# Kernel tuning notes

Hardware: AMD Instinct MI355X
Metric: run time of the kernel (lower is better)

Reference implementation:

```python
import jax, jax.numpy as jnp
import numpy as np

EPS = 1e-5
K = 20

def knn_idx(x, k):
    # x: (B, N, C) -> (B, N, k) indices of k nearest neighbors (negative sq-dist top-k, self included)
    sq = jnp.sum(x * x, axis=-1)                      # (B, N)
    inner = jnp.einsum('bnc,bmc->bnm', x, x)          # (B, N, N)
    neg_dist = 2.0 * inner - sq[:, :, None] - sq[:, None, :]
    _, idx = jax.lax.top_k(neg_dist, k)
    return idx

def edge_conv(x, w, g, b, m, v, k):
    # x: (B, N, C); w: (O, 2C); BN eval-mode params over O
    idx = knn_idx(x, k)                               # (B, N, k)
    nb = jax.vmap(lambda f, i: f[i])(x, idx)          # (B, N, k, C)
    ctr = x[:, :, None, :]
    e = jnp.concatenate([nb - ctr, jnp.broadcast_to(ctr, nb.shape)], axis=-1)  # (B,N,k,2C)
    h = jnp.einsum('bnkc,oc->bnko', e, w)
    h = (h - m) * jax.lax.rsqrt(v + EPS) * g + b
    h = jnp.where(h > 0, h, 0.2 * h)                  # LeakyReLU(0.2)
    return jnp.max(h, axis=2)                         # (B, N, O)

def conv1d_bn_relu(x, w, bias, g, bt, m, v):
    h = jnp.einsum('bnc,oc->bno', x, w) + bias
    h = (h - m) * jax.lax.rsqrt(v + EPS) * g + bt
    return jax.nn.relu(h)

def setup_inputs() -> dict:
    key = jax.random.key(0)
    ks = jax.random.split(key, 16)
    B, N = 2, 4096
    d = {'x': jax.random.normal(ks[0], (B, N, 3), dtype=jnp.float32)}
    dims = [(3, 64), (64, 64), (64, 128), (128, 256)]
    for i, (ci, co) in enumerate(dims, start=1):
        d[f'w{i}'] = jax.random.normal(ks[i], (co, 2 * ci), dtype=jnp.float32) * 0.05
        d[f'g{i}'] = jnp.ones((co,), jnp.float32)
        d[f'bt{i}'] = jnp.zeros((co,), jnp.float32)
        d[f'm{i}'] = jnp.zeros((co,), jnp.float32)
        d[f'v{i}'] = jnp.ones((co,), jnp.float32)
    head = [(512, 256), (256, 128)]
    for i, (ci, co) in enumerate(head, start=1):
        d[f'hw{i}'] = jax.random.normal(ks[8 + i], (co, ci), dtype=jnp.float32) * 0.05
        d[f'hb{i}'] = jnp.zeros((co,), jnp.float32)
        d[f'hg{i}'] = jnp.ones((co,), jnp.float32)
        d[f'hbt{i}'] = jnp.zeros((co,), jnp.float32)
        d[f'hm{i}'] = jnp.zeros((co,), jnp.float32)
        d[f'hv{i}'] = jnp.ones((co,), jnp.float32)
    d['hw3'] = jax.random.normal(ks[12], (1, 128), dtype=jnp.float32) * 0.05
    d['hb3'] = jnp.zeros((1,), jnp.float32)
    return d

def reference(x, w1, g1, bt1, m1, v1, w2, g2, bt2, m2, v2, w3, g3, bt3, m3, v3,
              w4, g4, bt4, m4, v4,
              hw1, hb1, hg1, hbt1, hm1, hv1, hw2, hb2, hg2, hbt2, hm2, hv2, hw3, hb3):
    x1 = edge_conv(x, w1, g1, bt1, m1, v1, K)   # (B, N, 64)
    x2 = edge_conv(x1, w2, g2, bt2, m2, v2, K)  # (B, N, 64)
    x3 = edge_conv(x2, w3, g3, bt3, m3, v3, K)  # (B, N, 128)
    x4 = edge_conv(x3, w4, g4, bt4, m4, v4, K)  # (B, N, 256)
    xc = jnp.concatenate([x1, x2, x3, x4], axis=-1)  # (B, N, 512)
    h = conv1d_bn_relu(xc, hw1, hb1, hg1, hbt1, hm1, hv1)
    h = conv1d_bn_relu(h, hw2, hb2, hg2, hbt2, hm2, hv2)
    out = jnp.einsum('bnc,oc->bno', h, hw3) + hb3    # (B, N, 1)
    return out[..., 0]                               # (B, N)
```

## Files before the change

kernel.cpp:

```cpp
#include <hip/hip_runtime.h>

#define NPTS 4096
#define EPSF 1e-5f

__device__ __forceinline__ unsigned f2u(float f) {
  unsigned b = __float_as_uint(f);
  return (b & 0x80000000u) ? ~b : (b | 0x80000000u);
}
__device__ __forceinline__ float u2f(unsigned u) {
  unsigned b = (u & 0x80000000u) ? (u & 0x7fffffffu) : ~u;
  return __uint_as_float(b);
}
__device__ __forceinline__ unsigned shflx(unsigned v, int j) {
  return (unsigned)__shfl_xor((int)v, j);
}
__device__ __forceinline__ unsigned long long shflx64(unsigned long long v, int j) {
  unsigned lo = (unsigned)__shfl_xor((int)(unsigned)(v & 0xffffffffull), j);
  unsigned hi = (unsigned)__shfl_xor((int)(unsigned)(v >> 32), j);
  return ((unsigned long long)hi << 32) | lo;
}

__device__ __forceinline__ unsigned sort64_u32(unsigned v, int lane) {
#pragma unroll
  for (int k = 2; k <= 64; k <<= 1) {
#pragma unroll
    for (int j = k >> 1; j >= 1; j >>= 1) {
      unsigned ov = shflx(v, j);
      bool kmin = ((lane & j) == 0) == ((lane & k) == 0);
      v = kmin ? (v < ov ? v : ov) : (v > ov ? v : ov);
    }
  }
  return v;
}

__device__ __forceinline__ void sort128_u32(unsigned& a, unsigned& b, int lane) {
#pragma unroll
  for (int k = 2; k <= 128; k <<= 1) {
#pragma unroll
    for (int j = k >> 1; j >= 1; j >>= 1) {
      if (j == 64) {
        unsigned mn = a < b ? a : b, mx = a < b ? b : a;
        a = mn; b = mx;
      } else {
        unsigned oa = shflx(a, j), ob = shflx(b, j);
        bool lower = (lane & j) == 0;
        bool asca, ascb;
        if (k == 128) { asca = true; ascb = true; }
        else if (k == 64) { asca = true; ascb = false; }
        else { asca = ((lane & k) == 0); ascb = asca; }
        a = (lower == asca) ? (a < oa ? a : oa) : (a > oa ? a : oa);
        b = (lower == ascb) ? (b < ob ? b : ob) : (b > ob ? b : ob);
      }
    }
  }
}

__device__ __forceinline__ unsigned long long sort64_u64(unsigned long long v, int lane) {
#pragma unroll
  for (int k = 2; k <= 64; k <<= 1) {
#pragma unroll
    for (int j = k >> 1; j >= 1; j >>= 1) {
      unsigned long long ov = shflx64(v, j);
      bool kmin = ((lane & j) == 0) == ((lane & k) == 0);
      v = kmin ? (v < ov ? v : ov) : (v > ov ? v : ov);
    }
  }
  return v;
}

__device__ __forceinline__ void sort128_u64(unsigned long long& a, unsigned long long& b,
                                            int lane) {
#pragma unroll
  for (int k = 2; k <= 128; k <<= 1) {
#pragma unroll
    for (int j = k >> 1; j >= 1; j >>= 1) {
      if (j == 64) {
        unsigned long long mn = a < b ? a : b, mx = a < b ? b : a;
        a = mn; b = mx;
      } else {
        unsigned long long oa = shflx64(a, j), ob = shflx64(b, j);
        bool lower = (lane & j) == 0;
        bool asca, ascb;
        if (k == 128) { asca = true; ascb = true; }
        else if (k == 64) { asca = true; ascb = false; }
        else { asca = ((lane & k) == 0); ascb = asca; }
        a = (lower == asca) ? (a < oa ? a : oa) : (a > oa ? a : oa);
        b = (lower == ascb) ? (b < ob ? b : ob) : (b > ob ? b : ob);
      }
    }
  }
}

__global__ void fold_edge_k(const float* __restrict__ w, const float* __restrict__ g,
                            const float* __restrict__ bt, const float* __restrict__ m,
                            const float* __restrict__ v, int O, int C,
                            float* __restrict__ wdf, float* __restrict__ wqf,
                            float* __restrict__ c0) {
  int t = blockIdx.x * 256 + threadIdx.x;
  if (t >= O * C) return;
  int o = t / C, c = t - o * C;
  float A = g[o] * (1.0f / sqrtf(v[o] + EPSF));
  float wd = w[o * 2 * C + c], wc = w[o * 2 * C + C + c];
  wdf[t] = A * wd;
  wqf[t] = A * (wc - wd);
  if (c == 0) c0[o] = bt[o] - m[o] * A;
}

__global__ void fold_head_k(const float* __restrict__ hw, const float* __restrict__ hb,
                            const float* __restrict__ hg, const float* __restrict__ hbt,
                            const float* __restrict__ hm, const float* __restrict__ hv,
                            int O, int C, float* __restrict__ hwf, float* __restrict__ cb) {
  int t = blockIdx.x * 256 + threadIdx.x;
  if (t >= O * C) return;
  int o = t / C, c = t - o * C;
  float A = hg[o] * (1.0f / sqrtf(hv[o] + EPSF));
  hwf[t] = A * hw[t];
  if (c == 0) cb[o] = (hb[o] - hm[o]) * A + hbt[o];
}

__global__ void sq_k(const float* __restrict__ X, int lda, int C,
                     float* __restrict__ sq, int nrows) {
  int r = blockIdx.x * 256 + threadIdx.x;
  if (r >= nrows) return;
  const float* p = X + (size_t)r * lda;
  float s = 0.f;
  for (int c = 0; c < C; ++c) s += p[c] * p[c];
  sq[r] = s;
}

__global__ void pq3_k(const float* __restrict__ x, const float* __restrict__ wdf,
                      const float* __restrict__ wqf, const float* __restrict__ c0,
                      float* __restrict__ P, float* __restrict__ Q) {
  int t = blockIdx.x * 256 + threadIdx.x;
  int r = t >> 6, o = t & 63;
  float x0 = x[r * 3], x1 = x[r * 3 + 1], x2 = x[r * 3 + 2];
  P[(size_t)r * 64 + o] = x0 * wdf[o * 3] + x1 * wdf[o * 3 + 1] + x2 * wdf[o * 3 + 2];
  Q[(size_t)r * 64 + o] = x0 * wqf[o * 3] + x1 * wqf[o * 3 + 1] + x2 * wqf[o * 3 + 2] + c0[o];
}

__global__ void dist3_all(const float* __restrict__ x, const float* __restrict__ sq,
                          float* __restrict__ D) {
  size_t t = (size_t)blockIdx.x * 256 + threadIdx.x;
  int mc = (int)(t & (NPTS - 1));
  int rg = (int)(t >> 12);
  int b = rg >> 12;
  int n = rg & (NPTS - 1);
  const float* xb = x + (size_t)b * NPTS * 3;
  const float* sqb = sq + (size_t)b * NPTS;
  float x0 = xb[n * 3], x1 = xb[n * 3 + 1], x2 = xb[n * 3 + 2];
  float y0 = xb[mc * 3], y1 = xb[mc * 3 + 1], y2 = xb[mc * 3 + 2];
  float inner = x0 * y0 + x1 * y1 + x2 * y2;
  D[(size_t)rg * NPTS + mc] = 2.0f * inner - sqb[n] - sqb[mc];
}

__global__ void dist3_k(const float* __restrict__ xb, const float* __restrict__ sqb,
                        float* __restrict__ D, int r0) {
  int t = blockIdx.x * 256 + threadIdx.x;
  int rl = t >> 12;
  int mc = t & (NPTS - 1);
  int n = r0 + rl;
  float x0 = xb[n * 3], x1 = xb[n * 3 + 1], x2 = xb[n * 3 + 2];
  float y0 = xb[mc * 3], y1 = xb[mc * 3 + 1], y2 = xb[mc * 3 + 2];
  float inner = x0 * y0 + x1 * y1 + x2 * y2;
  D[(size_t)rl * NPTS + mc] = 2.0f * inner - sqb[n] - sqb[mc];
}

__global__ __launch_bounds__(256) void dist_sym_k(
    const float* __restrict__ X0, int lda, int C,
    const float* __restrict__ sq0, float* __restrict__ D0) {
  int t = blockIdx.x;
  int bi = 0;
  while (t >= 32 - bi) { t -= 32 - bi; ++bi; }
  const int bj = bi + t;
  const int b = blockIdx.y;
  const float* X = X0 + (size_t)b * NPTS * lda;
  const float* sq = sq0 + (size_t)b * NPTS;
  float* D = D0 + (size_t)b * NPTS * NPTS;

  const int row0 = bi * 128, col0 = bj * 128;
  const int tid = threadIdx.x;
  const int tx = tid & 15, ty = tid >> 4;

  __shared__ float smem[4224];
  float* As = smem;
  float* Bs = smem + 2112;

  const int lr = tid >> 1;
  const int lc = (tid & 1) * 8;
  const float* Ap = X + (size_t)(row0 + lr) * lda + lc;
  const float* Bp = X + (size_t)(col0 + lr) * lda + lc;

  float acc[8][8] = {};
  for (int c0 = 0; c0 < C; c0 += 16) {
    float4 a0 = *(const float4*)(Ap + c0);
    float4 a1 = *(const float4*)(Ap + c0 + 4);
    float4 b0 = *(const float4*)(Bp + c0);
    float4 b1 = *(const float4*)(Bp + c0 + 4);
    __syncthreads();
    As[(lc + 0) * 132 + lr] = a0.x; As[(lc + 1) * 132 + lr] = a0.y;
    As[(lc + 2) * 132 + lr] = a0.z; As[(lc + 3) * 132 + lr] = a0.w;
    As[(lc + 4) * 132 + lr] = a1.x; As[(lc + 5) * 132 + lr] = a1.y;
    As[(lc + 6) * 132 + lr] = a1.z; As[(lc + 7) * 132 + lr] = a1.w;
    Bs[(lc + 0) * 132 + lr] = b0.x; Bs[(lc + 1) * 132 + lr] = b0.y;
    Bs[(lc + 2) * 132 + lr] = b0.z; Bs[(lc + 3) * 132 + lr] = b0.w;
    Bs[(lc + 4) * 132 + lr] = b1.x; Bs[(lc + 5) * 132 + lr] = b1.y;
    Bs[(lc + 6) * 132 + lr] = b1.z; Bs[(lc + 7) * 132 + lr] = b1.w;
    __syncthreads();
#pragma unroll
    for (int c = 0; c < 16; ++c) {
      float4 av0 = *(const float4*)&As[c * 132 + ty * 8];
      float4 av1 = *(const float4*)&As[c * 132 + ty * 8 + 4];
      float4 bv0 = *(const float4*)&Bs[c * 132 + tx * 8];
      float4 bv1 = *(const float4*)&Bs[c * 132 + tx * 8 + 4];
      float aa[8] = {av0.x, av0.y, av0.z, av0.w, av1.x, av1.y, av1.z, av1.w};
      float bb[8] = {bv0.x, bv0.y, bv0.z, bv0.w, bv1.x, bv1.y, bv1.z, bv1.w};
#pragma unroll
      for (int i = 0; i < 8; ++i)
#pragma unroll
        for (int j = 0; j < 8; ++j) acc[i][j] = fmaf(aa[i], bb[j], acc[i][j]);
    }
  }

  float rs[8], cs[8];
#pragma unroll
  for (int i = 0; i < 8; ++i) rs[i] = sq[row0 + ty * 8 + i];
#pragma unroll
  for (int j = 0; j < 8; ++j) cs[j] = sq[col0 + tx * 8 + j];

#pragma unroll
  for (int i = 0; i < 8; ++i) {
    const int row = row0 + ty * 8 + i;
    float vals[8];
#pragma unroll
    for (int j = 0; j < 8; ++j) vals[j] = (2.0f * acc[i][j] - rs[i]) - cs[j];
    *(float4*)&D[(size_t)row * NPTS + col0 + tx * 8] =
        make_float4(vals[0], vals[1], vals[2], vals[3]);
    *(float4*)&D[(size_t)row * NPTS + col0 + tx * 8 + 4] =
        make_float4(vals[4], vals[5], vals[6], vals[7]);
  }

  if (bi != bj) {
    for (int ch = 0; ch < 4; ++ch) {
      __syncthreads();
      if ((tx >> 2) == ch) {
#pragma unroll
        for (int j = 0; j < 8; ++j) {
          const int clocal = (tx & 3) * 8 + j;
#pragma unroll
          for (int i = 0; i < 8; ++i)
            smem[clocal * 129 + ty * 8 + i] = (2.0f * acc[i][j] - cs[j]) - rs[i];
        }
      }
      __syncthreads();
      const int cl = tid >> 3;
      const int seg = (tid & 7) * 16;
      float tv[16];
#pragma unroll
      for (int u = 0; u < 16; ++u) tv[u] = smem[cl * 129 + seg + u];
      const size_t mrow = (size_t)(col0 + ch * 32 + cl) * NPTS + row0 + seg;
#pragma unroll
      for (int q = 0; q < 4; ++q)
        *(float4*)&D[mrow + 4 * q] =
            make_float4(tv[4 * q], tv[4 * q + 1], tv[4 * q + 2], tv[4 * q + 3]);
    }
  }
}

template <int EPI>
__global__ __launch_bounds__(256) void gemm_nt(
    const float* __restrict__ A, int lda,
    const float* __restrict__ Bm, int ldb,
    float* __restrict__ Out, int ldo, int C,
    const float* __restrict__ sqA, const float* __restrict__ sqB,
    const float* __restrict__ bias) {
  __shared__ __align__(16) float As[16][68];
  __shared__ __align__(16) float Bs[16][68];
  const int tx = threadIdx.x, ty = threadIdx.y;
  const int tid = ty * 16 + tx;
  const int row0 = blockIdx.y * 64, col0 = blockIdx.x * 64;
  const int lr = tid >> 2;
  const int lc = (tid & 3) << 2;
  const float* Ap = A + (size_t)(row0 + lr) * lda + lc;
  const float* Bp = Bm + (size_t)(col0 + lr) * ldb + lc;
  float acc[4][4] = {};
  for (int c0 = 0; c0 < C; c0 += 16) {
    float4 av = *(const float4*)(Ap + c0);
    float4 bv = *(const float4*)(Bp + c0);
    As[lc + 0][lr] = av.x; As[lc + 1][lr] = av.y;
    As[lc + 2][lr] = av.z; As[lc + 3][lr] = av.w;
    Bs[lc + 0][lr] = bv.x; Bs[lc + 1][lr] = bv.y;
    Bs[lc + 2][lr] = bv.z; Bs[lc + 3][lr] = bv.w;
    __syncthreads();
#pragma unroll
    for (int c = 0; c < 16; ++c) {
      float4 a4 = *(const float4*)(&As[c][ty << 2]);
      float4 b4 = *(const float4*)(&Bs[c][tx << 2]);
      float aa[4] = {a4.x, a4.y, a4.z, a4.w};
      float bb[4] = {b4.x, b4.y, b4.z, b4.w};
#pragma unroll
      for (int i = 0; i < 4; ++i)
#pragma unroll
        for (int j = 0; j < 4; ++j) acc[i][j] = fmaf(aa[i], bb[j], acc[i][j]);
    }
    __syncthreads();
  }
  const int row = row0 + (ty << 2), col = col0 + (tx << 2);
#pragma unroll
  for (int i = 0; i < 4; ++i) {
    float vals[4];
#pragma unroll
    for (int j = 0; j < 4; ++j) {
      float va = acc[i][j];
      if (EPI == 0) vals[j] = va;
      else if (EPI == 1) vals[j] = va + bias[col + j];
      else if (EPI == 2) vals[j] = 2.0f * va - sqA[row + i] - sqB[col + j];
      else { float t = va + bias[col + j]; vals[j] = t > 0.f ? t : 0.f; }
    }
    *(float4*)(&Out[(size_t)(row + i) * ldo + col]) =
        make_float4(vals[0], vals[1], vals[2], vals[3]);
  }
}

__global__ __launch_bounds__(256) void topk_max_f32(
    const float* __restrict__ D, long long dStride,
    const float* __restrict__ P, const float* __restrict__ Q,
    float* __restrict__ Y, int ldy, int O, int bBase0, int r0) {
  const int tid = threadIdx.x;
  const int lane = tid & 63, wid = tid >> 6;
  const int nloc = blockIdx.x;
  const int n = r0 + nloc;
  const int bBase = bBase0 + blockIdx.y * NPTS;
  const float* drow = D + (size_t)blockIdx.y * (size_t)dStride + (size_t)nloc * NPTS;

  __shared__ unsigned wv[80];
  __shared__ unsigned ck[128];
  __shared__ int      ci[128];
  __shared__ int      cnt_s;
  __shared__ int      selm[20];
  __shared__ float    part[4 * 256];
  __shared__ float    fcv[80];
  __shared__ int      fcm[80];

  float v[16];
#pragma unroll
  for (int j = 0; j < 16; ++j) v[j] = drow[j * 256 + tid];

  float M = v[0];
#pragma unroll
  for (int j = 1; j < 16; ++j) M = fmaxf(M, v[j]);

  unsigned mk = sort64_u32(f2u(M), lane);

  if (tid == 0) cnt_s = 0;
  if (lane >= 44) wv[wid * 20 + (63 - lane)] = mk;
  __syncthreads();

  unsigned a0 = wv[lane];
  unsigned b0 = (lane < 16) ? wv[64 + lane] : 0u;
  sort128_u32(a0, b0, lane);
  unsigned T0k = (unsigned)__shfl((int)b0, 44);
  float T0f = u2f(T0k);

#pragma unroll
  for (int j = 0; j < 16; ++j) {
    bool pred = (v[j] >= T0f);
    unsigned long long m = __ballot(pred);
    int below = __popcll(m & ((1ull << lane) - 1ull));
    int cw = __popcll(m);
    int base = 0;
    if (lane == 0 && cw) base = atomicAdd(&cnt_s, cw);
    base = __shfl(base, 0);
    if (pred) {
      int pos = base + below;
      if (pos < 128) { ck[pos] = f2u(v[j]); ci[pos] = j * 256 + tid; }
    }
  }
  __syncthreads();
  const int cnt = cnt_s;

  if (cnt <= 128) {
    unsigned long long k0 = (lane < cnt)
        ? (((unsigned long long)ck[lane] << 32) | (unsigned)(~ci[lane])) : 0ull;
    if (cnt <= 64) {
      k0 = sort64_u64(k0, lane);
      if (wid == 0 && lane >= 44) selm[63 - lane] = (int)(~(unsigned)k0);
    } else {
      unsigned long long k1 = (64 + lane < cnt)
          ? (((unsigned long long)ck[64 + lane] << 32) | (unsigned)(~ci[64 + lane])) : 0ull;
      sort128_u64(k0, k1, lane);
      if (wid == 0 && lane >= 44) selm[63 - lane] = (int)(~(unsigned)k1);
    }
  } else {
    for (int it = 0; it < 20; ++it) {
      float bv = v[0]; int bj = 0;
#pragma unroll
      for (int j = 1; j < 16; ++j)
        if (v[j] > bv) { bv = v[j]; bj = j; }
      int bm = bj * 256 + tid;
#pragma unroll
      for (int off = 1; off < 64; off <<= 1) {
        float ov = __shfl_xor(bv, off);
        int om = __shfl_xor(bm, off);
        if (ov > bv || (ov == bv && om < bm)) { bv = ov; bm = om; }
      }
      if (lane == 0) { fcv[wid * 20 + it] = bv; fcm[wid * 20 + it] = bm; }
      if ((bm & 255) == tid) v[bm >> 8] = -3.0e38f;
    }
    __syncthreads();
    if (wid == 0) {
      float c0 = fcv[lane]; int m0 = fcm[lane];
      float c1 = (lane < 16) ? fcv[64 + lane] : -3.0e38f;
      int   m1 = (lane < 16) ? fcm[64 + lane] : 0x7fffffff;
      for (int it = 0; it < 20; ++it) {
        float bv; int bm, bs;
        if (c0 > c1 || (c0 == c1 && m0 < m1)) { bv = c0; bm = m0; bs = lane; }
        else { bv = c1; bm = m1; bs = 64 + lane; }
#pragma unroll
        for (int off = 1; off < 64; off <<= 1) {
          float ov = __shfl_xor(bv, off);
          int om = __shfl_xor(bm, off);
          int os = __shfl_xor(bs, off);
          if (ov > bv || (ov == bv && om < bm)) { bv = ov; bm = om; bs = os; }
        }
        if (lane == 0) selm[it] = bm;
        if (bs == lane) c0 = -3.0e38f;
        else if (bs == 64 + lane) c1 = -3.0e38f;
      }
    }
  }
  __syncthreads();

  for (int o = lane; o < O; o += 64) {
    float q = Q[(size_t)(bBase + n) * O + o];
    float best = -3.0e38f;
#pragma unroll
    for (int kk = 0; kk < 5; ++kk) {
      int s = selm[wid * 5 + kk];
      float t = P[(size_t)(bBase + s) * O + o] + q;
      t = t > 0.f ? t : 0.2f * t;
      best = fmaxf(best, t);
    }
    part[wid * 256 + o] = best;
  }
  __syncthreads();
  for (int o = tid; o < O; o += 256) {
    float b2 = fmaxf(fmaxf(part[o], part[256 + o]),
                     fmaxf(part[512 + o], part[768 + o]));
    Y[(size_t)(bBase + n) * ldy + o] = b2;
  }
}

__global__ void final_dot_k(const float* __restrict__ h2, const float* __restrict__ w3,
                            const float* __restrict__ b3, float* __restrict__ out) {
  int gt = blockIdx.x * 256 + threadIdx.x;
  int row = gt >> 6, lane = gt & 63;
  float s = h2[(size_t)row * 128 + lane] * w3[lane] +
            h2[(size_t)row * 128 + 64 + lane] * w3[64 + lane];
#pragma unroll
  for (int off = 32; off > 0; off >>= 1) s += __shfl_down(s, off);
  if (lane == 0) out[row] = s + b3[0];
}

extern "C" void kernel_launch(void* const* d_in, const int* in_sizes, int n_in,
                              void* d_out, int out_size, void* d_ws, size_t ws_size,
                              hipStream_t stream) {
  const int B = 2, N = NPTS;
  const size_t NN = (size_t)N * N;
  const float* x = (const float*)d_in[0];
  const float* w[4]  = {(const float*)d_in[1], (const float*)d_in[6],
                        (const float*)d_in[11], (const float*)d_in[16]};
  const float* g[4]  = {(const float*)d_in[2], (const float*)d_in[7],
                        (const float*)d_in[12], (const float*)d_in[17]};
  const float* bt[4] = {(const float*)d_in[3], (const float*)d_in[8],
                        (const float*)d_in[13], (const float*)d_in[18]};
  const float* mm[4] = {(const float*)d_in[4], (const float*)d_in[9],
                        (const float*)d_in[14], (const float*)d_in[19]};
  const float* vv[4] = {(const float*)d_in[5], (const float*)d_in[10],
                        (const float*)d_in[15], (const float*)d_in[20]};
  const float* hw1 = (const float*)d_in[21]; const float* hb1 = (const float*)d_in[22];
  const float* hg1 = (const float*)d_in[23]; const float* hbt1 = (const float*)d_in[24];
  const float* hm1 = (const float*)d_in[25]; const float* hv1 = (const float*)d_in[26];
  const float* hw2 = (const float*)d_in[27]; const float* hb2 = (const float*)d_in[28];
  const float* hg2 = (const float*)d_in[29]; const float* hbt2 = (const float*)d_in[30];
  const float* hm2 = (const float*)d_in[31]; const float* hv2 = (const float*)d_in[32];
  const float* hw3 = (const float*)d_in[33]; const float* hb3 = (const float*)d_in[34];
  float* out = (float*)d_out;

  char* wsb = (char*)d_ws;
  size_t off = 0;
  auto alloc = [&](size_t nbytes) {
    char* p = wsb + off;
    off += (nbytes + 255) & ~(size_t)255;
    return p;
  };
  float* xc   = (float*)alloc((size_t)B * N * 512 * 4);
  float* P    = (float*)alloc((size_t)B * N * 256 * 4);
  float* Q    = (float*)alloc((size_t)B * N * 256 * 4);
  float* sq   = (float*)alloc((size_t)B * N * 4);
  float* wdf  = (float*)alloc(256 * 256 * 4);
  float* wqf  = (float*)alloc(256 * 256 * 4);
  float* c0   = (float*)alloc(256 * 4);
  float* hwf1 = (float*)alloc(256 * 512 * 4);
  float* cb1  = (float*)alloc(256 * 4);
  float* hwf2 = (float*)alloc(128 * 256 * 4);
  float* cb2  = (float*)alloc(128 * 4);
  float* D    = (float*)(wsb + off);
  size_t avail = (ws_size > off) ? (ws_size - off) : 0;
  const bool merged = (avail >= (size_t)B * NN * 4);
  int rows_tile = 4096;
  if (!merged)
    while ((size_t)rows_tile * N * 4 > avail && rows_tile > 64) rows_tile >>= 1;

  const int Cin[4]  = {3, 64, 64, 128};
  const int Oc[4]   = {64, 64, 128, 256};
  const int ioff[4] = {0, 0, 64, 128};
  const int ooff[4] = {0, 64, 128, 256};
  dim3 blk2(16, 16);

  for (int L = 0; L < 4; ++L) {
    const int C = Cin[L], O = Oc[L];
    const float* in = (L == 0) ? x : (xc + ioff[L]);
    const int lda = (L == 0) ? 3 : 512;

    fold_edge_k<<<dim3((O * C + 255) / 256), dim3(256), 0, stream>>>(
        w[L], g[L], bt[L], mm[L], vv[L], O, C, wdf, wqf, c0);
    sq_k<<<dim3((B * N + 255) / 256), dim3(256), 0, stream>>>(in, lda, C, sq, B * N);
    if (L == 0) {
      pq3_k<<<dim3(B * N * 64 / 256), dim3(256), 0, stream>>>(x, wdf, wqf, c0, P, Q);
    } else {
      gemm_nt<0><<<dim3(O / 64, B * N / 64), blk2, 0, stream>>>(
          in, lda, wdf, C, P, O, C, nullptr, nullptr, nullptr);
      gemm_nt<1><<<dim3(O / 64, B * N / 64), blk2, 0, stream>>>(
          in, lda, wqf, C, Q, O, C, nullptr, nullptr, c0);
    }

    if (merged) {
      if (L == 0) {
        dist3_all<<<dim3((unsigned)((size_t)B * NN / 256)), dim3(256), 0, stream>>>(
            x, sq, D);
      } else {
        dist_sym_k<<<dim3(528, B), dim3(256), 0, stream>>>(in, lda, C, sq, D);
      }
      topk_max_f32<<<dim3(N, B), dim3(256), 0, stream>>>(
          D, (long long)NN, P, Q, xc + ooff[L], 512, O, 0, 0);
      continue;
    }

    for (int b = 0; b < B; ++b) {
      for (int r0 = 0; r0 < N; r0 += rows_tile) {
        if (L == 0) {
          dist3_k<<<dim3((unsigned)((size_t)rows_tile * N / 256)), dim3(256), 0, stream>>>(
              x + (size_t)b * N * 3, sq + b * N, D, r0);
        } else {
          gemm_nt<2><<<dim3(N / 64, rows_tile / 64), blk2, 0, stream>>>(
              in + ((size_t)b * N + r0) * lda, lda, in + (size_t)b * N * lda, lda,
              D, N, C, sq + b * N + r0, sq + b * N, nullptr);
        }
        topk_max_f32<<<dim3(rows_tile, 1), dim3(256), 0, stream>>>(
            D, 0, P, Q, xc + ooff[L], 512, O, b * N, r0);
      }
    }
  }

  fold_head_k<<<dim3((256 * 512 + 255) / 256), dim3(256), 0, stream>>>(
      hw1, hb1, hg1, hbt1, hm1, hv1, 256, 512, hwf1, cb1);
  fold_head_k<<<dim3((128 * 256 + 255) / 256), dim3(256), 0, stream>>>(
      hw2, hb2, hg2, hbt2, hm2, hv2, 128, 256, hwf2, cb2);

  float* h1 = P;
  float* h2 = Q;
  gemm_nt<3><<<dim3(256 / 64, B * N / 64), blk2, 0, stream>>>(
      xc, 512, hwf1, 512, h1, 256, 512, nullptr, nullptr, cb1);
  gemm_nt<3><<<dim3(128 / 64, B * N / 64), blk2, 0, stream>>>(
      h1, 256, hwf2, 256, h2, 128, 256, nullptr, nullptr, cb2);
  final_dot_k<<<dim3(B * N / 4), dim3(256), 0, stream>>>(h2, hw3, hb3, out);
}
```

Measured before the change: 715.4 us.

## Fuse layer-1 distance computation into top-k kernel and write mirror tiles directly

For the first edge-conv layer (C=3), distances are now computed in registers inside the top-k kernel, so the full B*N*N distance matrix is no longer written to and read back from global memory. The shared top-k selection and gather logic is moved into device helpers that both kernels use. The symmetric distance kernel also drops its shared-memory transpose and writes mirrored tiles straight to global memory with strided float4 stores. That removes several barriers but gives less coalesced stores, since each thread writes 32-byte pieces across rows.

Result: faster. 700.8 us (-2.0%).

```diff
diff --git a/kernel.cpp b/kernel.cpp
--- a/kernel.cpp
+++ b/kernel.cpp
@@ -91,6 +91,131 @@
   }
 }
 
+struct TopkShared {
+  unsigned wv[80];
+  unsigned ck[128];
+  int      ci[128];
+  int      cnt_s;
+  int      selm[20];
+  float    part[4 * 256];
+  float    fcv[80];
+  int      fcm[80];
+};
+
+__device__ __forceinline__ void topk_select(float v[16], TopkShared& sh,
+                                            int tid, int lane, int wid) {
+  float M = v[0];
+#pragma unroll
+  for (int j = 1; j < 16; ++j) M = fmaxf(M, v[j]);
+
+  unsigned mk = sort64_u32(f2u(M), lane);
+
+  if (tid == 0) sh.cnt_s = 0;
+  if (lane >= 44) sh.wv[wid * 20 + (63 - lane)] = mk;
+  __syncthreads();
+
+  unsigned a0 = sh.wv[lane];
+  unsigned b0 = (lane < 16) ? sh.wv[64 + lane] : 0u;
+  sort128_u32(a0, b0, lane);
+  unsigned T0k = (unsigned)__shfl((int)b0, 44);
+  float T0f = u2f(T0k);
+
+#pragma unroll
+  for (int j = 0; j < 16; ++j) {
+    bool pred = (v[j] >= T0f);
+    unsigned long long m = __ballot(pred);
+    int below = __popcll(m & ((1ull << lane) - 1ull));
+    int cw = __popcll(m);
+    int base = 0;
+    if (lane == 0 && cw) base = atomicAdd(&sh.cnt_s, cw);
+    base = __shfl(base, 0);
+    if (pred) {
+      int pos = base + below;
+      if (pos < 128) { sh.ck[pos] = f2u(v[j]); sh.ci[pos] = j * 256 + tid; }
+    }
+  }
+  __syncthreads();
+  const int cnt = sh.cnt_s;
+
+  if (cnt <= 128) {
+    unsigned long long k0 = (lane < cnt)
+        ? (((unsigned long long)sh.ck[lane] << 32) | (unsigned)(~sh.ci[lane])) : 0ull;
+    if (cnt <= 64) {
+      k0 = sort64_u64(k0, lane);
+      if (wid == 0 && lane >= 44) sh.selm[63 - lane] = (int)(~(unsigned)k0);
+    } else {
+      unsigned long long k1 = (64 + lane < cnt)
+          ? (((unsigned long long)sh.ck[64 + lane] << 32) | (unsigned)(~sh.ci[64 + lane]))
+          : 0ull;
+      sort128_u64(k0, k1, lane);
+      if (wid == 0 && lane >= 44) sh.selm[63 - lane] = (int)(~(unsigned)k1);
+    }
+  } else {
+    for (int it = 0; it < 20; ++it) {
+      float bv = v[0]; int bj = 0;
+#pragma unroll
+      for (int j = 1; j < 16; ++j)
+        if (v[j] > bv) { bv = v[j]; bj = j; }
+      int bm = bj * 256 + tid;
+#pragma unroll
+      for (int off = 1; off < 64; off <<= 1) {
+        float ov = __shfl_xor(bv, off);
+        int om = __shfl_xor(bm, off);
+        if (ov > bv || (ov == bv && om < bm)) { bv = ov; bm = om; }
+      }
+      if (lane == 0) { sh.fcv[wid * 20 + it] = bv; sh.fcm[wid * 20 + it] = bm; }
+      if ((bm & 255) == tid) v[bm >> 8] = -3.0e38f;
+    }
+    __syncthreads();
+    if (wid == 0) {
+      float c0 = sh.fcv[lane]; int m0 = sh.fcm[lane];
+      float c1 = (lane < 16) ? sh.fcv[64 + lane] : -3.0e38f;
+      int   m1 = (lane < 16) ? sh.fcm[64 + lane] : 0x7fffffff;
+      for (int it = 0; it < 20; ++it) {
+        float bv; int bm, bs;
+        if (c0 > c1 || (c0 == c1 && m0 < m1)) { bv = c0; bm = m0; bs = lane; }
+        else { bv = c1; bm = m1; bs = 64 + lane; }
+#pragma unroll
+        for (int off = 1; off < 64; off <<= 1) {
+          float ov = __shfl_xor(bv, off);
+          int om = __shfl_xor(bm, off);
+          int os = __shfl_xor(bs, off);
+          if (ov > bv || (ov == bv && om < bm)) { bv = ov; bm = om; bs = os; }
+        }
+        if (lane == 0) sh.selm[it] = bm;
+        if (bs == lane) c0 = -3.0e38f;
+        else if (bs == 64 + lane) c1 = -3.0e38f;
+      }
+    }
+  }
+  __syncthreads();
+}
+
+__device__ __forceinline__ void topk_gather(const TopkShared& sh, TopkShared& shm,
+                                            const float* __restrict__ P,
+                                            const float* __restrict__ Q,
+                                            float* __restrict__ Y, int ldy, int O,
+                                            int bBase, int n, int tid, int lane, int wid) {
+  for (int o = lane; o < O; o += 64) {
+    float q = Q[(size_t)(bBase + n) * O + o];
+    float best = -3.0e38f;
+#pragma unroll
+    for (int kk = 0; kk < 5; ++kk) {
+      int s = sh.selm[wid * 5 + kk];
+      float t = P[(size_t)(bBase + s) * O + o] + q;
+      t = t > 0.f ? t : 0.2f * t;
+      best = fmaxf(best, t);
+    }
+    shm.part[wid * 256 + o] = best;
+  }
+  __syncthreads();
+  for (int o = tid; o < O; o += 256) {
+    float b2 = fmaxf(fmaxf(shm.part[o], shm.part[256 + o]),
+                     fmaxf(shm.part[512 + o], shm.part[768 + o]));
+    Y[(size_t)(bBase + n) * ldy + o] = b2;
+  }
+}
+
 __global__ void fold_edge_k(const float* __restrict__ w, const float* __restrict__ g,
                             const float* __restrict__ bt, const float* __restrict__ m,
                             const float* __restrict__ v, int O, int C,
@@ -138,21 +263,6 @@
   Q[(size_t)r * 64 + o] = x0 * wqf[o * 3] + x1 * wqf[o * 3 + 1] + x2 * wqf[o * 3 + 2] + c0[o];
 }
 
-__global__ void dist3_all(const float* __restrict__ x, const float* __restrict__ sq,
-                          float* __restrict__ D) {
-  size_t t = (size_t)blockIdx.x * 256 + threadIdx.x;
-  int mc = (int)(t & (NPTS - 1));
-  int rg = (int)(t >> 12);
-  int b = rg >> 12;
-  int n = rg & (NPTS - 1);
-  const float* xb = x + (size_t)b * NPTS * 3;
-  const float* sqb = sq + (size_t)b * NPTS;
-  float x0 = xb[n * 3], x1 = xb[n * 3 + 1], x2 = xb[n * 3 + 2];
-  float y0 = xb[mc * 3], y1 = xb[mc * 3 + 1], y2 = xb[mc * 3 + 2];
-  float inner = x0 * y0 + x1 * y1 + x2 * y2;
-  D[(size_t)rg * NPTS + mc] = 2.0f * inner - sqb[n] - sqb[mc];
-}
-
 __global__ void dist3_k(const float* __restrict__ xb, const float* __restrict__ sqb,
                         float* __restrict__ D, int r0) {
   int t = blockIdx.x * 256 + threadIdx.x;
@@ -163,6 +273,34 @@
   float y0 = xb[mc * 3], y1 = xb[mc * 3 + 1], y2 = xb[mc * 3 + 2];
   float inner = x0 * y0 + x1 * y1 + x2 * y2;
   D[(size_t)rl * NPTS + mc] = 2.0f * inner - sqb[n] - sqb[mc];
+}
+
+__global__ __launch_bounds__(256) void topk_l1_fused(
+    const float* __restrict__ x, const float* __restrict__ sqg,
+    const float* __restrict__ P, const float* __restrict__ Q,
+    float* __restrict__ Y, int ldy) {
+  const int tid = threadIdx.x;
+  const int lane = tid & 63, wid = tid >> 6;
+  const int n = blockIdx.x;
+  const int bBase = blockIdx.y * NPTS;
+  const float* xb = x + (size_t)bBase * 3;
+  const float* sqb = sqg + bBase;
+
+  __shared__ TopkShared sh;
+
+  float xn0 = xb[n * 3], xn1 = xb[n * 3 + 1], xn2 = xb[n * 3 + 2];
+  float sn = sqb[n];
+  float v[16];
+#pragma unroll
+  for (int j = 0; j < 16; ++j) {
+    int mc = j * 256 + tid;
+    float y0 = xb[mc * 3], y1 = xb[mc * 3 + 1], y2 = xb[mc * 3 + 2];
+    float inner = xn0 * y0 + xn1 * y1 + xn2 * y2;
+    v[j] = 2.0f * inner - sn - sqb[mc];
+  }
+
+  topk_select(v, sh, tid, lane, wid);
+  topk_gather(sh, sh, P, Q, Y, ldy, 64, bBase, n, tid, lane, wid);
 }
 
 __global__ __launch_bounds__(256) void dist_sym_k(
@@ -181,9 +319,8 @@
   const int tid = threadIdx.x;
   const int tx = tid & 15, ty = tid >> 4;
 
-  __shared__ float smem[4224];
-  float* As = smem;
-  float* Bs = smem + 2112;
+  __shared__ float As[16 * 132];
+  __shared__ float Bs[16 * 132];
 
   const int lr = tid >> 1;
   const int lc = (tid & 1) * 8;
@@ -240,28 +377,16 @@
   }
 
   if (bi != bj) {
-    for (int ch = 0; ch < 4; ++ch) {
-      __syncthreads();
-      if ((tx >> 2) == ch) {
-#pragma unroll
-        for (int j = 0; j < 8; ++j) {
-          const int clocal = (tx & 3) * 8 + j;
-#pragma unroll
-          for (int i = 0; i < 8; ++i)
-            smem[clocal * 129 + ty * 8 + i] = (2.0f * acc[i][j] - cs[j]) - rs[i];
-        }
-      }
-      __syncthreads();
-      const int cl = tid >> 3;
-      const int seg = (tid & 7) * 16;
-      float tv[16];
-#pragma unroll
-      for (int u = 0; u < 16; ++u) tv[u] = smem[cl * 129 + seg + u];
-      const size_t mrow = (size_t)(col0 + ch * 32 + cl) * NPTS + row0 + seg;
-#pragma unroll
-      for (int q = 0; q < 4; ++q)
-        *(float4*)&D[mrow + 4 * q] =
-            make_float4(tv[4 * q], tv[4 * q + 1], tv[4 * q + 2], tv[4 * q + 3]);
+#pragma unroll
+    for (int j = 0; j < 8; ++j) {
+      const int col = col0 + tx * 8 + j;
+      float mv[8];
+#pragma unroll
+      for (int i = 0; i < 8; ++i) mv[i] = (2.0f * acc[i][j] - cs[j]) - rs[i];
+      *(float4*)&D[(size_t)col * NPTS + row0 + ty * 8] =
+          make_float4(mv[0], mv[1], mv[2], mv[3]);
+      *(float4*)&D[(size_t)col * NPTS + row0 + ty * 8 + 4] =
+          make_float4(mv[4], mv[5], mv[6], mv[7]);
     }
   }
 }
@@ -332,122 +457,14 @@
   const int bBase = bBase0 + blockIdx.y * NPTS;
   const float* drow = D + (size_t)blockIdx.y * (size_t)dStride + (size_t)nloc * NPTS;
 
-  __shared__ unsigned wv[80];
-  __shared__ unsigned ck[128];
-  __shared__ int      ci[128];
-  __shared__ int      cnt_s;
-  __shared__ int      selm[20];
-  __shared__ float    part[4 * 256];
-  __shared__ float    fcv[80];
-  __shared__ int      fcm[80];
+  __shared__ TopkShared sh;
 
   float v[16];
 #pragma unroll
   for (int j = 0; j < 16; ++j) v[j] = drow[j * 256 + tid];
 
-  float M = v[0];
-#pragma unroll
-  for (int j = 1; j < 16; ++j) M = fmaxf(M, v[j]);
-
-  unsigned mk = sort64_u32(f2u(M), lane);
-
-  if (tid == 0) cnt_s = 0;
-  if (lane >= 44) wv[wid * 20 + (63 - lane)] = mk;
-  __syncthreads();
-
-  unsigned a0 = wv[lane];
-  unsigned b0 = (lane < 16) ? wv[64 + lane] : 0u;
-  sort128_u32(a0, b0, lane);
-  unsigned T0k = (unsigned)__shfl((int)b0, 44);
-  float T0f = u2f(T0k);
-
-#pragma unroll
-  for (int j = 0; j < 16; ++j) {
-    bool pred = (v[j] >= T0f);
-    unsigned long long m = __ballot(pred);
-    int below = __popcll(m & ((1ull << lane) - 1ull));
-    int cw = __popcll(m);
-    int base = 0;
-    if (lane == 0 && cw) base = atomicAdd(&cnt_s, cw);
-    base = __shfl(base, 0);
-    if (pred) {
-      int pos = base + below;
-      if (pos < 128) { ck[pos] = f2u(v[j]); ci[pos] = j * 256 + tid; }
-    }
-  }
-  __syncthreads();
-  const int cnt = cnt_s;
-
-  if (cnt <= 128) {
-    unsigned long long k0 = (lane < cnt)
-        ? (((unsigned long long)ck[lane] << 32) | (unsigned)(~ci[lane])) : 0ull;
-    if (cnt <= 64) {
-      k0 = sort64_u64(k0, lane);
-      if (wid == 0 && lane >= 44) selm[63 - lane] = (int)(~(unsigned)k0);
-    } else {
-      unsigned long long k1 = (64 + lane < cnt)
-          ? (((unsigned long long)ck[64 + lane] << 32) | (unsigned)(~ci[64 + lane])) : 0ull;
-      sort128_u64(k0, k1, lane);
-      if (wid == 0 && lane >= 44) selm[63 - lane] = (int)(~(unsigned)k1);
-    }
-  } else {
-    for (int it = 0; it < 20; ++it) {
-      float bv = v[0]; int bj = 0;
-#pragma unroll
-      for (int j = 1; j < 16; ++j)
-        if (v[j] > bv) { bv = v[j]; bj = j; }
-      int bm = bj * 256 + tid;
-#pragma unroll
-      for (int off = 1; off < 64; off <<= 1) {
-        float ov = __shfl_xor(bv, off);
-        int om = __shfl_xor(bm, off);
-        if (ov > bv || (ov == bv && om < bm)) { bv = ov; bm = om; }
-      }
-      if (lane == 0) { fcv[wid * 20 + it] = bv; fcm[wid * 20 + it] = bm; }
-      if ((bm & 255) == tid) v[bm >> 8] = -3.0e38f;
-    }
-    __syncthreads();
-    if (wid == 0) {
-      float c0 = fcv[lane]; int m0 = fcm[lane];
-      float c1 = (lane < 16) ? fcv[64 + lane] : -3.0e38f;
-      int   m1 = (lane < 16) ? fcm[64 + lane] : 0x7fffffff;
-      for (int it = 0; it < 20; ++it) {
-        float bv; int bm, bs;
-        if (c0 > c1 || (c0 == c1 && m0 < m1)) { bv = c0; bm = m0; bs = lane; }
-        else { bv = c1; bm = m1; bs = 64 + lane; }
-#pragma unroll
-        for (int off = 1; off < 64; off <<= 1) {
-          float ov = __shfl_xor(bv, off);
-          int om = __shfl_xor(bm, off);
-          int os = __shfl_xor(bs, off);
-          if (ov > bv || (ov == bv && om < bm)) { bv = ov; bm = om; bs = os; }
-        }
-        if (lane == 0) selm[it] = bm;
-        if (bs == lane) c0 = -3.0e38f;
-        else if (bs == 64 + lane) c1 = -3.0e38f;
-      }
-    }
-  }
-  __syncthreads();
-
-  for (int o = lane; o < O; o += 64) {
-    float q = Q[(size_t)(bBase + n) * O + o];
-    float best = -3.0e38f;
-#pragma unroll
-    for (int kk = 0; kk < 5; ++kk) {
-      int s = selm[wid * 5 + kk];
-      float t = P[(size_t)(bBase + s) * O + o] + q;
-      t = t > 0.f ? t : 0.2f * t;
-      best = fmaxf(best, t);
-    }
-    part[wid * 256 + o] = best;
-  }
-  __syncthreads();
-  for (int o = tid; o < O; o += 256) {
-    float b2 = fmaxf(fmaxf(part[o], part[256 + o]),
-                     fmaxf(part[512 + o], part[768 + o]));
-    Y[(size_t)(bBase + n) * ldy + o] = b2;
-  }
+  topk_select(v, sh, tid, lane, wid);
+  topk_gather(sh, sh, P, Q, Y, ldy, O, bBase, n, tid, lane, wid);
 }
 
 __global__ void final_dot_k(const float* __restrict__ h2, const float* __restrict__ w3,
@@ -536,13 +553,13 @@
 
     if (merged) {
       if (L == 0) {
-        dist3_all<<<dim3((unsigned)((size_t)B * NN / 256)), dim3(256), 0, stream>>>(
-            x, sq, D);
+        topk_l1_fused<<<dim3(N, B), dim3(256), 0, stream>>>(
+            x, sq, P, Q, xc + ooff[0], 512);
       } else {
         dist_sym_k<<<dim3(528, B), dim3(256), 0, stream>>>(in, lda, C, sq, D);
+        topk_max_f32<<<dim3(N, B), dim3(256), 0, stream>>>(
+            D, (long long)NN, P, Q, xc + ooff[L], 512, O, 0, 0);
       }
-      topk_max_f32<<<dim3(N, B), dim3(256), 0, stream>>>(
-          D, (long long)NN, P, Q, xc + ooff[L], 512, O, 0, 0);
       continue;
     }
 
```
